# Performance work log

Hardware: AMD Instinct MI355X
Metric: run time of the kernel (lower is better)

The kernel has to match this reference:

```python
import jax, jax.numpy as jnp
import numpy as np

H = 1024      # hidden_size
I = 2 * H     # intermediate_size (expand_factor=2)
N = 16        # ssm_state_size
K = 4         # conv_kernel
BATCH = 2
SEQ = 2048


def setup_inputs() -> dict:
    key = jax.random.key(0)
    k = jax.random.split(key, 6)
    x = jax.random.normal(k[0], (BATCH, SEQ, H), dtype=jnp.float32)
    # nn.Linear default init ~ U(-1/sqrt(fan_in), 1/sqrt(fan_in)); scale is fine for a reference
    W_in = jax.random.normal(k[1], (2 * I, H), dtype=jnp.float32) / np.sqrt(H)
    conv_w = jax.random.normal(k[2], (I, 1, K), dtype=jnp.float32) / np.sqrt(K)
    W_x = jax.random.normal(k[3], (2 * N + 1, I), dtype=jnp.float32) / np.sqrt(I)
    A_log = jax.random.normal(k[4], (I, N), dtype=jnp.float32)
    D = jnp.ones((I,), dtype=jnp.float32)
    W_out = jax.random.normal(k[5], (H, I), dtype=jnp.float32) / np.sqrt(I)
    return {"x": x, "W_in": W_in, "conv_w": conv_w, "W_x": W_x,
            "A_log": A_log, "D": D, "W_out": W_out}


def reference(x, W_in, conv_w, W_x, A_log, D, W_out):
    xz = jnp.einsum('bsh,ih->bsi', x, W_in)
    xp, z = jnp.split(xz, 2, axis=-1)
    # depthwise causal conv1d: pad left K-1 (torch pads both sides then slices [:S])
    xc = jax.lax.conv_general_dilated(
        xp.transpose(0, 2, 1),           # (B, I, S)
        conv_w,                          # (I, 1, K) = OIH with groups=I
        window_strides=(1,),
        padding=[(K - 1, 0)],
        feature_group_count=I,
        dimension_numbers=('NCH', 'OIH', 'NCH'),
    ).transpose(0, 2, 1)                 # (B, S, I)
    xc = jax.nn.silu(xc)
    # x_proj -> delta (1), B (N), C (N)
    xproj = jnp.einsum('bsi,pi->bsp', xc, W_x)   # (B,S,2N+1)
    delta = jax.nn.softplus(xproj[..., :1])       # (B,S,1)
    Bmat = xproj[..., 1:1 + N]                    # (B,S,N)
    Cmat = xproj[..., 1 + N:]                     # (B,S,N)
    A = -jnp.exp(A_log)                           # (I,N)
    # decay/states broadcast-reduce: (B,S,I,N) intermediates reduced over N
    decay = jnp.exp(delta[..., None] * A[None, None])            # (B,S,I,N)
    states = xc[..., None] * Bmat[:, :, None, :] * decay          # (B,S,I,N)
    y = jnp.sum(states * Cmat[:, :, None, :], axis=-1)            # (B,S,I)
    y = y + xc * D[None, None, :]
    return jnp.einsum('bsi,hi->bsh', y * jax.nn.silu(z), W_out)
```

## Files before the change

kernel.cpp:

```cpp
#include <hip/hip_runtime.h>

#define LOG2E 1.4426950408889634f

__device__ __forceinline__ float b2f(unsigned short u) {
    unsigned int v = ((unsigned int)u) << 16;
    return __builtin_bit_cast(float, v);
}
__device__ __forceinline__ unsigned short f2b(float f) {
    unsigned int u = __builtin_bit_cast(unsigned int, f);
    u += 0x7fffu + ((u >> 16) & 1u);
    return (unsigned short)(u >> 16);
}
__device__ __forceinline__ float fexp(float x) {
    return __builtin_amdgcn_exp2f(x * LOG2E);
}
__device__ __forceinline__ float silu_f(float x) {
    return x * __builtin_amdgcn_rcpf(1.0f + fexp(-x));
}

typedef const __attribute__((address_space(1))) unsigned int* gas_t;
typedef __attribute__((address_space(3))) unsigned int* las_t;
__device__ __forceinline__ void gl2lds16(const unsigned short* g, unsigned short* l) {
    __builtin_amdgcn_global_load_lds((gas_t)(const void*)g, (las_t)(void*)l, 16, 0, 0);
}

__global__ __launch_bounds__(256) void cvt_bf16_k(const float* __restrict__ in,
                                                  unsigned short* __restrict__ out,
                                                  int n4) {
    int i = blockIdx.x * 256 + threadIdx.x;
    if (i >= n4) return;
    float4 v = ((const float4*)in)[i];
    *(ushort4*)(out + (size_t)i * 4) = make_ushort4(f2b(v.x), f2b(v.y), f2b(v.z), f2b(v.w));
}

typedef __bf16 bf16x8 __attribute__((ext_vector_type(8)));
typedef float  fx4    __attribute__((ext_vector_type(4)));
typedef int    ix4    __attribute__((ext_vector_type(4)));
union FragU { ix4 i; bf16x8 b; };

template <bool OUT_BF16>
__global__ __launch_bounds__(256) void gemm_bt(const unsigned short* __restrict__ A,
                                               const unsigned short* __restrict__ B,
                                               void* __restrict__ C, int N, int K) {
    __shared__ __align__(16) unsigned short sA[128 * 64];
    __shared__ __align__(16) unsigned short sB[128 * 64];
    const int tid  = threadIdx.x;
    const int lane = tid & 63, wave = tid >> 6;
    const int bm = blockIdx.y * 128, bn = blockIdx.x * 128;
    const int wm = (wave >> 1) * 64, wn = (wave & 1) * 64;
    const int row16 = lane & 15, quad = lane >> 4;
    const int srow = lane >> 3;
    const int sc16 = (lane & 7) ^ srow;
    const unsigned short* gA = A + (size_t)(bm + wave * 32 + srow) * K + sc16 * 8;
    const unsigned short* gB = B + (size_t)(bn + wave * 32 + srow) * K + sc16 * 8;
    unsigned short* lA = sA + (wave * 4) * 512;
    unsigned short* lB = sB + (wave * 4) * 512;
    fx4 acc[4][4] = {};

    for (int kt = 0; kt < K; kt += 64) {
#pragma unroll
        for (int it = 0; it < 4; ++it) {
            gl2lds16(gA + (size_t)it * 8 * K + kt, lA + it * 512);
            gl2lds16(gB + (size_t)it * 8 * K + kt, lB + it * 512);
        }
        __syncthreads();
#pragma unroll
        for (int kk = 0; kk < 64; kk += 32) {
            FragU af[4], bf[4];
#pragma unroll
            for (int t = 0; t < 4; ++t) {
                int ra = wm + t * 16 + row16;
                af[t].i = *(const ix4*)(sA + ra * 64 + ((quad + (kk >> 3)) ^ (ra & 7)) * 8);
            }
#pragma unroll
            for (int t = 0; t < 4; ++t) {
                int rb = wn + t * 16 + row16;
                bf[t].i = *(const ix4*)(sB + rb * 64 + ((quad + (kk >> 3)) ^ (rb & 7)) * 8);
            }
#pragma unroll
            for (int tm = 0; tm < 4; ++tm)
#pragma unroll
                for (int tn = 0; tn < 4; ++tn)
                    acc[tm][tn] = __builtin_amdgcn_mfma_f32_16x16x32_bf16(
                        af[tm].b, bf[tn].b, acc[tm][tn], 0, 0, 0);
        }
        __syncthreads();
    }
#pragma unroll
    for (int tm = 0; tm < 4; ++tm) {
        int row0 = bm + wm + tm * 16 + quad * 4;
#pragma unroll
        for (int tn = 0; tn < 4; ++tn) {
            int col = bn + wn + tn * 16 + row16;
#pragma unroll
            for (int r = 0; r < 4; ++r) {
                float v = acc[tm][tn][r];
                if (OUT_BF16)
                    ((unsigned short*)C)[(size_t)(row0 + r) * N + col] = f2b(v);
                else
                    ((float*)C)[(size_t)(row0 + r) * N + col] = v;
            }
        }
    }
}

__global__ __launch_bounds__(256) void conv_silu_k(const unsigned short* __restrict__ xz,
                                                   const float* __restrict__ cw,
                                                   float* __restrict__ xc,
                                                   unsigned short* __restrict__ xcb) {
    const int ti = threadIdx.x & 31, tm = threadIdx.x >> 5;
    const int i0 = blockIdx.x * 256 + ti * 8;
    const int m  = blockIdx.y * 8 + tm;
    const int s  = m & 2047;
    float w[8][4];
    const float4* cw4 = (const float4*)cw;
#pragma unroll
    for (int j = 0; j < 8; ++j) {
        float4 t = cw4[i0 + j];
        w[j][0] = t.x; w[j][1] = t.y; w[j][2] = t.z; w[j][3] = t.w;
    }
    float acc[8] = {0, 0, 0, 0, 0, 0, 0, 0};
#pragma unroll
    for (int k = 0; k < 4; ++k) {
        int sr = s - 3 + k;
        if (sr >= 0) {
            const unsigned short* p = xz + (size_t)(m - 3 + k) * 4096 + i0;
            ushort4 a = *(const ushort4*)p;
            ushort4 b = *(const ushort4*)(p + 4);
            float v[8] = {b2f(a.x), b2f(a.y), b2f(a.z), b2f(a.w),
                          b2f(b.x), b2f(b.y), b2f(b.z), b2f(b.w)};
#pragma unroll
            for (int j = 0; j < 8; ++j) acc[j] += v[j] * w[j][k];
        }
    }
    float o[8];
#pragma unroll
    for (int j = 0; j < 8; ++j) o[j] = silu_f(acc[j]);
    float* q = xc + (size_t)m * 2048 + i0;
    *(float4*)q       = make_float4(o[0], o[1], o[2], o[3]);
    *(float4*)(q + 4) = make_float4(o[4], o[5], o[6], o[7]);
    unsigned short* qb = xcb + (size_t)m * 2048 + i0;
    *(ushort4*)qb       = make_ushort4(f2b(o[0]), f2b(o[1]), f2b(o[2]), f2b(o[3]));
    *(ushort4*)(qb + 4) = make_ushort4(f2b(o[4]), f2b(o[5]), f2b(o[6]), f2b(o[7]));
}

__global__ __launch_bounds__(256) void xproj_mfma(const unsigned short* __restrict__ xcb,
                                                  const unsigned short* __restrict__ wxb,
                                                  float* __restrict__ dg) {
    __shared__ float sX[4][16][49];
    const int tid = threadIdx.x;
    const int lane = tid & 63, wave = tid >> 6;
    const int row16 = lane & 15, quad = lane >> 4;
    const int m0 = blockIdx.x * 16;
    fx4 acc[3] = {};
    const unsigned short* ap = xcb + (size_t)(m0 + row16) * 2048 + wave * 512 + quad * 8;
    const unsigned short* bp = wxb + (size_t)row16 * 2048 + wave * 512 + quad * 8;
#pragma unroll 4
    for (int kk = 0; kk < 512; kk += 32) {
        FragU a, b0, b1, b2;
        a.i  = *(const ix4*)(ap + kk);
        b0.i = *(const ix4*)(bp + kk);
        b1.i = *(const ix4*)(bp + 16 * 2048 + kk);
        b2.i = *(const ix4*)(bp + 32 * 2048 + kk);
        acc[0] = __builtin_amdgcn_mfma_f32_16x16x32_bf16(a.b, b0.b, acc[0], 0, 0, 0);
        acc[1] = __builtin_amdgcn_mfma_f32_16x16x32_bf16(a.b, b1.b, acc[1], 0, 0, 0);
        acc[2] = __builtin_amdgcn_mfma_f32_16x16x32_bf16(a.b, b2.b, acc[2], 0, 0, 0);
    }
#pragma unroll
    for (int t = 0; t < 3; ++t)
#pragma unroll
        for (int r = 0; r < 4; ++r)
            sX[wave][quad * 4 + r][t * 16 + row16] = acc[t][r];
    __syncthreads();
    for (int idx = tid; idx < 272; idx += 256) {
        int rr = idx / 17, q = idx - rr * 17;
        float o;
        if (q == 0) {
            float v = sX[0][rr][0] + sX[1][rr][0] + sX[2][rr][0] + sX[3][rr][0];
            o = (v > 20.f) ? v : log1pf(fexp(v));
        } else {
            float bs = sX[0][rr][q]      + sX[1][rr][q]      + sX[2][rr][q]      + sX[3][rr][q];
            float cs = sX[0][rr][q + 16] + sX[1][rr][q + 16] + sX[2][rr][q + 16] + sX[3][rr][q + 16];
            o = bs * cs;
        }
        dg[(size_t)(m0 + rr) * 17 + q] = o;
    }
}

__global__ __launch_bounds__(256) void ssm_pw_k(const unsigned short* __restrict__ xz,
                                                const float* __restrict__ xc,
                                                const float* __restrict__ dg,
                                                const float* __restrict__ Alog,
                                                const float* __restrict__ Dv,
                                                unsigned short* __restrict__ y2) {
    __shared__ float sa[64 * 19];
    __shared__ float sdg[32 * 17];
    const int tid = threadIdx.x;
    const int bi = blockIdx.x, bm = blockIdx.y;
    for (int t = tid; t < 1024; t += 256) {
        float a = Alog[bi * 1024 + t];
        int il = t >> 4, n = t & 15;
        sa[il * 19 + n] = -fexp(a) * LOG2E;
    }
    for (int t = tid; t < 544; t += 256) sdg[t] = dg[(size_t)bm * 32 * 17 + t];
    __syncthreads();
    const int t_i = tid & 7, t_m = tid >> 3;
    const int m  = bm * 32 + t_m;
    const int i0 = bi * 64 + t_i * 8;
    const float delta = sdg[t_m * 17];
    float G[16];
#pragma unroll
    for (int n = 0; n < 16; ++n) G[n] = sdg[t_m * 17 + 1 + n];
    const float* xcp = xc + (size_t)m * 2048 + i0;
    float4 xv0 = *(const float4*)xcp, xv1 = *(const float4*)(xcp + 4);
    const unsigned short* zp = xz + (size_t)m * 4096 + 2048 + i0;
    ushort4 zu0 = *(const ushort4*)zp, zu1 = *(const ushort4*)(zp + 4);
    float4 d0 = *(const float4*)(Dv + i0), d1 = *(const float4*)(Dv + i0 + 4);
    float xcv[8] = {xv0.x, xv0.y, xv0.z, xv0.w, xv1.x, xv1.y, xv1.z, xv1.w};
    float zv[8]  = {b2f(zu0.x), b2f(zu0.y), b2f(zu0.z), b2f(zu0.w),
                    b2f(zu1.x), b2f(zu1.y), b2f(zu1.z), b2f(zu1.w)};
    float dv[8]  = {d0.x, d0.y, d0.z, d0.w, d1.x, d1.y, d1.z, d1.w};
    unsigned short outv[8];
#pragma unroll
    for (int ii = 0; ii < 8; ++ii) {
        const float* ap = sa + (t_i * 8 + ii) * 19;
        float ssum = 0.f;
#pragma unroll
        for (int n = 0; n < 16; ++n)
            ssum += G[n] * __builtin_amdgcn_exp2f(delta * ap[n]);
        float y = xcv[ii] * (dv[ii] + ssum);
        outv[ii] = f2b(y * silu_f(zv[ii]));
    }
    unsigned short* q = y2 + (size_t)m * 2048 + i0;
    *(ushort4*)q       = make_ushort4(outv[0], outv[1], outv[2], outv[3]);
    *(ushort4*)(q + 4) = make_ushort4(outv[4], outv[5], outv[6], outv[7]);
}

extern "C" void kernel_launch(void* const* d_in, const int* in_sizes, int n_in,
                              void* d_out, int out_size, void* d_ws, size_t ws_size,
                              hipStream_t stream) {
    const float* x      = (const float*)d_in[0];
    const float* W_in   = (const float*)d_in[1];
    const float* conv_w = (const float*)d_in[2];
    const float* W_x    = (const float*)d_in[3];
    const float* A_log  = (const float*)d_in[4];
    const float* Dvec   = (const float*)d_in[5];
    const float* W_out  = (const float*)d_in[6];

    char* ws = (char*)d_ws;
    unsigned short* xb  = (unsigned short*)(ws);
    unsigned short* wib = (unsigned short*)(ws + 8388608);
    unsigned short* wob = (unsigned short*)(ws + 16777216);
    unsigned short* xz  = (unsigned short*)(ws + 20971520);
    float*          xcf = (float*)        (ws + 54525952);
    float*          dgp = (float*)        (ws + 88080384);
    unsigned short* y2  = (unsigned short*)(ws + 88358912);
    unsigned short* xcb = (unsigned short*)(ws + 105136128);
    unsigned short* wxb = (unsigned short*)(ws + 121913344);

    cvt_bf16_k<<<4096, 256, 0, stream>>>(x, xb, 1048576);
    cvt_bf16_k<<<4096, 256, 0, stream>>>(W_in, wib, 1048576);
    cvt_bf16_k<<<2048, 256, 0, stream>>>(W_out, wob, 524288);
    cvt_bf16_k<<<66, 256, 0, stream>>>(W_x, wxb, 16896);
    gemm_bt<true><<<dim3(32, 32), 256, 0, stream>>>(xb, wib, xz, 4096, 1024);
    conv_silu_k<<<dim3(8, 512), 256, 0, stream>>>(xz, conv_w, xcf, xcb);
    xproj_mfma<<<256, 256, 0, stream>>>(xcb, wxb, dgp);
    ssm_pw_k<<<dim3(32, 128), 256, 0, stream>>>(xz, xcf, dgp, A_log, Dvec, y2);
    gemm_bt<false><<<dim3(8, 32), 256, 0, stream>>>(y2, wob, (float*)d_out, 1024, 2048);
}
```

Baseline: 251.5 us.

## Merge conversion launches, drop fp32 conv output, add narrower output GEMM tile

The four bf16 conversion launches become one kernel that picks its source and destination by block index. The conv kernel stops writing the fp32 copy of the activated conv output, and the SSM kernel reads the bf16 copy instead, which cuts global write and read traffic. The final projection GEMM switches to a 128x64 tile so that 512 blocks run instead of 256, improving CU occupancy. Reading the conv output as bf16 slightly reduces precision in the pointwise step.

Result: faster. 233.1 us (-7.3%).

```diff
diff --git a/kernel.cpp b/kernel.cpp
--- a/kernel.cpp
+++ b/kernel.cpp
@@ -24,13 +24,24 @@
     __builtin_amdgcn_global_load_lds((gas_t)(const void*)g, (las_t)(void*)l, 16, 0, 0);
 }
 
-__global__ __launch_bounds__(256) void cvt_bf16_k(const float* __restrict__ in,
-                                                  unsigned short* __restrict__ out,
-                                                  int n4) {
-    int i = blockIdx.x * 256 + threadIdx.x;
-    if (i >= n4) return;
-    float4 v = ((const float4*)in)[i];
-    *(ushort4*)(out + (size_t)i * 4) = make_ushort4(f2b(v.x), f2b(v.y), f2b(v.z), f2b(v.w));
+__global__ __launch_bounds__(256) void cvt_all_k(const float* __restrict__ x,
+                                                 const float* __restrict__ W_in,
+                                                 const float* __restrict__ W_out,
+                                                 const float* __restrict__ W_x,
+                                                 unsigned short* __restrict__ xb,
+                                                 unsigned short* __restrict__ wib,
+                                                 unsigned short* __restrict__ wob,
+                                                 unsigned short* __restrict__ wxb) {
+    int b = blockIdx.x;
+    const float* src;
+    unsigned short* dst;
+    if (b < 4096)       { src = x;     dst = xb;  }
+    else if (b < 8192)  { src = W_in;  dst = wib; b -= 4096; }
+    else if (b < 10240) { src = W_out; dst = wob; b -= 8192; }
+    else                { src = W_x;   dst = wxb; b -= 10240; }
+    int i = b * 256 + threadIdx.x;
+    float4 v = ((const float4*)src)[i];
+    *(ushort4*)(dst + (size_t)i * 4) = make_ushort4(f2b(v.x), f2b(v.y), f2b(v.z), f2b(v.w));
 }
 
 typedef __bf16 bf16x8 __attribute__((ext_vector_type(8)));
@@ -104,9 +115,69 @@
     }
 }
 
+__global__ __launch_bounds__(256) void gemm_bt_n64(const unsigned short* __restrict__ A,
+                                                   const unsigned short* __restrict__ B,
+                                                   float* __restrict__ C, int N, int K) {
+    __shared__ __align__(16) unsigned short sA[128 * 64];
+    __shared__ __align__(16) unsigned short sB[64 * 64];
+    const int tid  = threadIdx.x;
+    const int lane = tid & 63, wave = tid >> 6;
+    const int bm = blockIdx.y * 128, bn = blockIdx.x * 64;
+    const int wm = wave * 32;
+    const int row16 = lane & 15, quad = lane >> 4;
+    const int srow = lane >> 3;
+    const int sc16 = (lane & 7) ^ srow;
+    const unsigned short* gA = A + (size_t)(bm + wave * 32 + srow) * K + sc16 * 8;
+    const unsigned short* gB = B + (size_t)(bn + wave * 16 + srow) * K + sc16 * 8;
+    unsigned short* lA = sA + (wave * 4) * 512;
+    unsigned short* lB = sB + (wave * 2) * 512;
+    fx4 acc[2][4] = {};
+
+    for (int kt = 0; kt < K; kt += 64) {
+#pragma unroll
+        for (int it = 0; it < 4; ++it)
+            gl2lds16(gA + (size_t)it * 8 * K + kt, lA + it * 512);
+#pragma unroll
+        for (int it = 0; it < 2; ++it)
+            gl2lds16(gB + (size_t)it * 8 * K + kt, lB + it * 512);
+        __syncthreads();
+#pragma unroll
+        for (int kk = 0; kk < 64; kk += 32) {
+            FragU af[2], bf[4];
+#pragma unroll
+            for (int t = 0; t < 2; ++t) {
+                int ra = wm + t * 16 + row16;
+                af[t].i = *(const ix4*)(sA + ra * 64 + ((quad + (kk >> 3)) ^ (ra & 7)) * 8);
+            }
+#pragma unroll
+            for (int t = 0; t < 4; ++t) {
+                int rb = t * 16 + row16;
+                bf[t].i = *(const ix4*)(sB + rb * 64 + ((quad + (kk >> 3)) ^ (rb & 7)) * 8);
+            }
+#pragma unroll
+            for (int tm = 0; tm < 2; ++tm)
+#pragma unroll
+                for (int tn = 0; tn < 4; ++tn)
+                    acc[tm][tn] = __builtin_amdgcn_mfma_f32_16x16x32_bf16(
+                        af[tm].b, bf[tn].b, acc[tm][tn], 0, 0, 0);
+        }
+        __syncthreads();
+    }
+#pragma unroll
+    for (int tm = 0; tm < 2; ++tm) {
+        int row0 = bm + wm + tm * 16 + quad * 4;
+#pragma unroll
+        for (int tn = 0; tn < 4; ++tn) {
+            int col = bn + tn * 16 + row16;
+#pragma unroll
+            for (int r = 0; r < 4; ++r)
+                C[(size_t)(row0 + r) * N + col] = acc[tm][tn][r];
+        }
+    }
+}
+
 __global__ __launch_bounds__(256) void conv_silu_k(const unsigned short* __restrict__ xz,
                                                    const float* __restrict__ cw,
-                                                   float* __restrict__ xc,
                                                    unsigned short* __restrict__ xcb) {
     const int ti = threadIdx.x & 31, tm = threadIdx.x >> 5;
     const int i0 = blockIdx.x * 256 + ti * 8;
@@ -133,15 +204,11 @@
             for (int j = 0; j < 8; ++j) acc[j] += v[j] * w[j][k];
         }
     }
-    float o[8];
-#pragma unroll
-    for (int j = 0; j < 8; ++j) o[j] = silu_f(acc[j]);
-    float* q = xc + (size_t)m * 2048 + i0;
-    *(float4*)q       = make_float4(o[0], o[1], o[2], o[3]);
-    *(float4*)(q + 4) = make_float4(o[4], o[5], o[6], o[7]);
     unsigned short* qb = xcb + (size_t)m * 2048 + i0;
-    *(ushort4*)qb       = make_ushort4(f2b(o[0]), f2b(o[1]), f2b(o[2]), f2b(o[3]));
-    *(ushort4*)(qb + 4) = make_ushort4(f2b(o[4]), f2b(o[5]), f2b(o[6]), f2b(o[7]));
+    *(ushort4*)qb       = make_ushort4(f2b(silu_f(acc[0])), f2b(silu_f(acc[1])),
+                                       f2b(silu_f(acc[2])), f2b(silu_f(acc[3])));
+    *(ushort4*)(qb + 4) = make_ushort4(f2b(silu_f(acc[4])), f2b(silu_f(acc[5])),
+                                       f2b(silu_f(acc[6])), f2b(silu_f(acc[7])));
 }
 
 __global__ __launch_bounds__(256) void xproj_mfma(const unsigned short* __restrict__ xcb,
@@ -188,7 +255,7 @@
 }
 
 __global__ __launch_bounds__(256) void ssm_pw_k(const unsigned short* __restrict__ xz,
-                                                const float* __restrict__ xc,
+                                                const unsigned short* __restrict__ xcb,
                                                 const float* __restrict__ dg,
                                                 const float* __restrict__ Alog,
                                                 const float* __restrict__ Dv,
@@ -211,12 +278,13 @@
     float G[16];
 #pragma unroll
     for (int n = 0; n < 16; ++n) G[n] = sdg[t_m * 17 + 1 + n];
-    const float* xcp = xc + (size_t)m * 2048 + i0;
-    float4 xv0 = *(const float4*)xcp, xv1 = *(const float4*)(xcp + 4);
+    const unsigned short* xcp = xcb + (size_t)m * 2048 + i0;
+    ushort4 xu0 = *(const ushort4*)xcp, xu1 = *(const ushort4*)(xcp + 4);
     const unsigned short* zp = xz + (size_t)m * 4096 + 2048 + i0;
     ushort4 zu0 = *(const ushort4*)zp, zu1 = *(const ushort4*)(zp + 4);
     float4 d0 = *(const float4*)(Dv + i0), d1 = *(const float4*)(Dv + i0 + 4);
-    float xcv[8] = {xv0.x, xv0.y, xv0.z, xv0.w, xv1.x, xv1.y, xv1.z, xv1.w};
+    float xcv[8] = {b2f(xu0.x), b2f(xu0.y), b2f(xu0.z), b2f(xu0.w),
+                    b2f(xu1.x), b2f(xu1.y), b2f(xu1.z), b2f(xu1.w)};
     float zv[8]  = {b2f(zu0.x), b2f(zu0.y), b2f(zu0.z), b2f(zu0.w),
                     b2f(zu1.x), b2f(zu1.y), b2f(zu1.z), b2f(zu1.w)};
     float dv[8]  = {d0.x, d0.y, d0.z, d0.w, d1.x, d1.y, d1.z, d1.w};
@@ -252,19 +320,15 @@
     unsigned short* wib = (unsigned short*)(ws + 8388608);
     unsigned short* wob = (unsigned short*)(ws + 16777216);
     unsigned short* xz  = (unsigned short*)(ws + 20971520);
-    float*          xcf = (float*)        (ws + 54525952);
-    float*          dgp = (float*)        (ws + 88080384);
-    unsigned short* y2  = (unsigned short*)(ws + 88358912);
-    unsigned short* xcb = (unsigned short*)(ws + 105136128);
-    unsigned short* wxb = (unsigned short*)(ws + 121913344);
-
-    cvt_bf16_k<<<4096, 256, 0, stream>>>(x, xb, 1048576);
-    cvt_bf16_k<<<4096, 256, 0, stream>>>(W_in, wib, 1048576);
-    cvt_bf16_k<<<2048, 256, 0, stream>>>(W_out, wob, 524288);
-    cvt_bf16_k<<<66, 256, 0, stream>>>(W_x, wxb, 16896);
+    float*          dgp = (float*)        (ws + 54525952);
+    unsigned short* y2  = (unsigned short*)(ws + 54804480);
+    unsigned short* xcb = (unsigned short*)(ws + 71581696);
+    unsigned short* wxb = (unsigned short*)(ws + 88358912);
+
+    cvt_all_k<<<10306, 256, 0, stream>>>(x, W_in, W_out, W_x, xb, wib, wob, wxb);
     gemm_bt<true><<<dim3(32, 32), 256, 0, stream>>>(xb, wib, xz, 4096, 1024);
-    conv_silu_k<<<dim3(8, 512), 256, 0, stream>>>(xz, conv_w, xcf, xcb);
+    conv_silu_k<<<dim3(8, 512), 256, 0, stream>>>(xz, conv_w, xcb);
     xproj_mfma<<<256, 256, 0, stream>>>(xcb, wxb, dgp);
-    ssm_pw_k<<<dim3(32, 128), 256, 0, stream>>>(xz, xcf, dgp, A_log, Dvec, y2);
-    gemm_bt<false><<<dim3(8, 32), 256, 0, stream>>>(y2, wob, (float*)d_out, 1024, 2048);
-}
+    ssm_pw_k<<<dim3(32, 128), 256, 0, stream>>>(xz, xcb, dgp, A_log, Dvec, y2);
+    gemm_bt_n64<<<dim3(16, 32), 256, 0, stream>>>(y2, wob, (float*)d_out, 1024, 2048);
+}
```
